# Kernel tuning notes

Hardware: AMD Instinct MI355X
Metric: run time of the kernel (lower is better)

## Reference

```python
import jax, jax.numpy as jnp
import numpy as np

B = 32768
N_INT = 32          # num_intruders
OWN_D = 3
INT_D = 7
ATTN_D = 128
HID = 256
OUT_D = 2
OBS_D = OWN_D + N_INT * INT_D  # 227
NEG_SLOPE = 0.2

def _lrelu(x):
    return jax.nn.leaky_relu(x, NEG_SLOPE)

def setup_inputs() -> dict:
    key = jax.random.key(0)
    ks = jax.random.split(key, 16)
    obs = jax.random.normal(ks[0], (B, OBS_D), dtype=jnp.float32)
    pad = jax.random.bernoulli(ks[1], 0.25, (B, N_INT))
    intr = obs[:, OWN_D:].reshape(B, N_INT, INT_D)
    intr = jnp.where(pad[:, :, None], 0.0, intr)
    obs = jnp.concatenate([obs[:, :OWN_D], intr.reshape(B, -1)], axis=1)
    def glorot(k, shape):
        fan_in, fan_out = shape[0], shape[-1]
        lim = jnp.sqrt(6.0 / (fan_in + fan_out))
        return jax.random.uniform(k, shape, jnp.float32, -lim, lim)
    return {
        "obs": obs,
        "own_W": glorot(ks[2], (OWN_D, ATTN_D)), "own_b": jnp.zeros((ATTN_D,), jnp.float32),
        "int_W": glorot(ks[3], (INT_D, ATTN_D)), "int_b": jnp.zeros((ATTN_D,), jnp.float32),
        "Wq": glorot(ks[4], (ATTN_D, ATTN_D)),
        "Wk": glorot(ks[5], (ATTN_D, ATTN_D)),
        "Wv": glorot(ks[6], (ATTN_D, ATTN_D)),
        "v_att": glorot(ks[7], (ATTN_D, 1))[:, 0],
        "proj_W": glorot(ks[8], (ATTN_D, ATTN_D)), "proj_b": jnp.zeros((ATTN_D,), jnp.float32),
        "h1_W": glorot(ks[9], (2 * ATTN_D, HID)), "h1_b": jnp.zeros((HID,), jnp.float32),
        "h2_W": glorot(ks[10], (HID, HID)), "h2_b": jnp.zeros((HID,), jnp.float32),
        "out_W": glorot(ks[11], (HID, OUT_D)), "out_b": jnp.zeros((OUT_D,), jnp.float32),
    }

def reference(obs, own_W, own_b, int_W, int_b, Wq, Wk, Wv, v_att,
              proj_W, proj_b, h1_W, h1_b, h2_W, h2_b, out_W, out_b):
    own = obs[:, :OWN_D]                                   # [B,3]
    intr = obs[:, OWN_D:OWN_D + N_INT * INT_D].reshape(-1, N_INT, INT_D)  # [B,N,7]
    own_e = _lrelu(own @ own_W + own_b)                    # [B,128]
    int_e = _lrelu(intr @ int_W + int_b)                   # [B,N,128]
    q = own_e @ Wq                                         # [B,128]
    k = int_e @ Wk                                         # [B,N,128]
    v = int_e @ Wv                                         # [B,N,128]
    energy = jnp.tanh(q[:, None, :] + k)                   # [B,N,128]
    scores = energy @ v_att                                # [B,N]
    is_padding = jnp.abs(intr).sum(axis=2) < 1e-6          # [B,N]
    scores = jnp.where(is_padding, -jnp.inf, scores)
    alpha = jax.nn.softmax(scores, axis=-1)
    alpha = jnp.nan_to_num(alpha, nan=0.0)
    ctx = jnp.einsum('bn,bnd->bd', alpha, v)               # [B,128]
    attn_vec = jnp.tanh(ctx @ proj_W + proj_b)             # [B,128]
    x = jnp.concatenate([own_e, attn_vec], axis=1)         # [B,256]
    x = _lrelu(x @ h1_W + h1_b)
    x = _lrelu(x @ h2_W + h2_b)
    return x @ out_W + out_b                               # [B,2]
```

## Files before the change

### kernel.cpp

```cpp
#include <hip/hip_runtime.h>
#include <hip/hip_bf16.h>
#include <math.h>

typedef _Float16 half2_t __attribute__((ext_vector_type(2)));
typedef _Float16 f16x8   __attribute__((ext_vector_type(8)));
typedef float    f32x4   __attribute__((ext_vector_type(4)));

constexpr int BATCH = 32768;
constexpr int NI   = 32;
constexpr int OWND = 3;
constexpr int INTD = 7;
constexpr int AD   = 128;
constexpr int HIDN = 256;
constexpr int OUTD = 2;
constexpr int OBSD = OWND + NI * INTD;
constexpr int IEPITCH = 68;
constexpr float C2L2E = 2.885390081777927f;

__device__ __forceinline__ half2_t u2h(unsigned u) { return __builtin_bit_cast(half2_t, u); }
__device__ __forceinline__ unsigned packf(float a, float b) {
    half2_t h = { (_Float16)a, (_Float16)b };
    return __builtin_bit_cast(unsigned, h);
}
__device__ __forceinline__ float lrelu(float x) { return fmaxf(x, 0.2f * x); }
__device__ __forceinline__ float exp2fast(float x) { return __builtin_amdgcn_exp2f(x); }
__device__ __forceinline__ float fast_tanh(float x) {
    float e = exp2fast(x * C2L2E);
    return 1.0f - 2.0f * __builtin_amdgcn_rcpf(e + 1.0f);
}

constexpr int UW_PWKQ = 0;
constexpr int UW_PWVF = 16384;
constexpr int UW_PPRF = 24576;
constexpr int UW_PIWF = 32768;
constexpr int UW_PH1F = 34816;
constexpr int UW_PH2F = 67584;
constexpr int UW_FULL = 100352;
constexpr size_t XBUF_U = (size_t)BATCH * (HIDN / 2);

__global__ __launch_bounds__(256) void pack_full(
    const float* __restrict__ Wq, const float* __restrict__ Wk,
    const float* __restrict__ Wv, const float* __restrict__ Pr,
    const float* __restrict__ IW, const float* __restrict__ IB,
    const float* __restrict__ H1, const float* __restrict__ H2,
    unsigned* __restrict__ dst)
{
    int u = blockIdx.x * 256 + threadIdx.x;
    if (u >= UW_FULL) return;
    if (u < 16384) {
        int f = u >> 8, kt = f >> 3, nt = f & 7;
        int idx = u & 255, lane = idx >> 2, w = idx & 3;
        int qd = lane >> 4, lo = lane & 15;
        const float* src = (kt < 4) ? Wk : Wq;
        int ktp = kt & 3;
        int r0 = 32 * ktp + 8 * qd + 2 * w, col = 16 * nt + lo;
        dst[u] = packf(src[r0 * 128 + col], src[(r0 + 1) * 128 + col]);
    } else if (u < 32768) {
        const float* src = (u < 24576) ? Wv : Pr;
        int i = (u - 16384) & 8191;
        int f = i >> 8, kt = f >> 3, nt = f & 7;
        int idx = i & 255, lane = idx >> 2, w = idx & 3;
        int qd = lane >> 4, lo = lane & 15;
        int r0 = 32 * kt + 8 * qd + 2 * w, col = 16 * nt + lo;
        dst[u] = packf(src[r0 * 128 + col], src[(r0 + 1) * 128 + col]);
    } else if (u < 34816) {
        int i = u - 32768;
        int nt = i >> 8;
        int idx = i & 255, lane = idx >> 2, w = idx & 3;
        int qd = lane >> 4, lo = lane & 15;
        int r0 = 8 * qd + 2 * w, col = 16 * nt + lo;
        float v0 = (r0 < INTD) ? IW[r0 * 128 + col] : 0.f;
        float v1 = (r0 + 1 < INTD) ? IW[(r0 + 1) * 128 + col]
                 : ((r0 + 1 == INTD) ? IB[col] : 0.f);
        dst[u] = packf(v0, v1);
    } else {
        int i = u - 34816;
        const float* src = (i < 32768) ? H1 : H2;
        i &= 32767;
        int f = i >> 8, nt = f >> 3, kt = f & 7;
        int idx = i & 255, lane = idx >> 2, w = idx & 3;
        int qd = lane >> 4, lo = lane & 15;
        int r0 = 32 * kt + 8 * qd + 2 * w, col = 16 * nt + lo;
        dst[u] = packf(src[r0 * 256 + col], src[(r0 + 1) * 256 + col]);
    }
}

__global__ __launch_bounds__(256) void qgemm(
    const float* __restrict__ obs, const float* __restrict__ own_W,
    const float* __restrict__ own_b, const unsigned* __restrict__ pWkqF,
    float* __restrict__ qall)
{
    const int wv = threadIdx.x >> 6;
    const int l  = threadIdx.x & 63;
    const int lo = l & 15, qd = l >> 4;
    const size_t row0 = (size_t)blockIdx.x * 64 + (size_t)wv * 16;

    __shared__ __align__(16) float    s_own[4][16][4];
    __shared__ __align__(16) unsigned s_oe[4][16 * 68];

    if (l < 16) {
        const float* orow = obs + (row0 + l) * OBSD;
        s_own[wv][l][0] = orow[0]; s_own[wv][l][1] = orow[1]; s_own[wv][l][2] = orow[2];
    }

    {
        const float x0 = s_own[wv][lo][0], x1 = s_own[wv][lo][1], x2 = s_own[wv][lo][2];
        #pragma unroll
        for (int jj = 0; jj < 8; jj++) {
            const int c4 = qd * 32 + jj * 4;
            float4 wb = *(const float4*)(own_b + c4);
            float4 w0 = *(const float4*)(own_W + 0 * AD + c4);
            float4 w1 = *(const float4*)(own_W + 1 * AD + c4);
            float4 w2 = *(const float4*)(own_W + 2 * AD + c4);
            float v0 = lrelu(wb.x + x0 * w0.x + x1 * w1.x + x2 * w2.x);
            float v1 = lrelu(wb.y + x0 * w0.y + x1 * w1.y + x2 * w2.y);
            float v2 = lrelu(wb.z + x0 * w0.z + x1 * w1.z + x2 * w2.z);
            float v3 = lrelu(wb.w + x0 * w0.w + x1 * w1.w + x2 * w2.w);
            s_oe[wv][lo * 68 + (c4 >> 1)]     = packf(v0, v1);
            s_oe[wv][lo * 68 + (c4 >> 1) + 1] = packf(v2, v3);
        }
    }

    f16x8 aE[4];
    #pragma unroll
    for (int kt = 0; kt < 4; kt++) {
        uint4 au = *(const uint4*)(&s_oe[wv][lo * 68 + 16 * kt + 4 * qd]);
        aE[kt] = __builtin_bit_cast(f16x8, au);
    }
    #pragma unroll
    for (int nt = 0; nt < 8; nt++) {
        f32x4 acc = {0.f, 0.f, 0.f, 0.f};
        #pragma unroll
        for (int kt = 0; kt < 4; kt++) {
            uint4 bu = *(const uint4*)(pWkqF + (((kt + 4) * 8 + nt) << 8) + (l << 2));
            acc = __builtin_amdgcn_mfma_f32_16x16x32_f16(aE[kt], __builtin_bit_cast(f16x8, bu), acc, 0, 0, 0);
        }
        #pragma unroll
        for (int r = 0; r < 4; r++)
            qall[(row0 + 4 * qd + r) * AD + 16 * nt + lo] = acc[r];
    }
}

__global__ __launch_bounds__(256) void attn(
    const float* __restrict__ obs,
    const float* __restrict__ own_W, const float* __restrict__ own_b,
    const unsigned* __restrict__ pIWF, const float* __restrict__ int_b,
    const unsigned* __restrict__ pWkqF, const float* __restrict__ v_att,
    const float* __restrict__ qall,
    unsigned* __restrict__ xbuf)
{
    const int wv = threadIdx.x >> 6;
    const int l  = threadIdx.x & 63;
    const int b  = blockIdx.x * 4 + wv;
    const int d0 = 2 * l;
    const int lo = l & 15, qd = l >> 4;
    const bool useQ = (qall != nullptr);

    __shared__ __align__(16) unsigned s_w[10240];
    __shared__ __align__(16) float    s_obs[4][OBSD];
    __shared__ __align__(16) unsigned s_ieb[4][NI * IEPITCH];
    __shared__ __align__(16) unsigned s_ownh[4][AD / 2];
    __shared__ __align__(16) float    s_sc[4][NI];

    if (useQ) {
        #pragma unroll
        for (int it = 0; it < 8; it++) {
            int idx = (threadIdx.x + it * 256) << 2;
            *(uint4*)(&s_w[idx]) = *(const uint4*)(pWkqF + idx);
        }
        #pragma unroll
        for (int it = 0; it < 2; it++) {
            int idx = (threadIdx.x + it * 256) << 2;
            *(uint4*)(&s_w[8192 + idx]) = *(const uint4*)(pIWF + idx);
        }
    }

    const float* orow = obs + (size_t)b * OBSD;
    for (int i = l; i < OBSD; i += 64) s_obs[wv][i] = orow[i];

    float oe0 = own_b[d0], oe1 = own_b[d0 + 1];
    #pragma unroll
    for (int j = 0; j < OWND; j++) {
        float x = s_obs[wv][j];
        oe0 += x * own_W[j * AD + d0];
        oe1 += x * own_W[j * AD + d0 + 1];
    }
    oe0 = lrelu(oe0); oe1 = lrelu(oe1);
    s_ownh[wv][l] = packf(oe0, oe1);

    int padf = 0;
    if (l < NI) {
        float su = 0.f;
        #pragma unroll
        for (int j = 0; j < INTD; j++) su += fabsf(s_obs[wv][OWND + l * INTD + j]);
        padf = (su < 1e-6f);
    }

    float qe[8];
    if (useQ) {
        const float* qrow = qall + (size_t)b * AD;
        #pragma unroll
        for (int nt = 0; nt < 8; nt++) qe[nt] = qrow[16 * nt + lo] * C2L2E;
    } else {
        #pragma unroll
        for (int nt = 0; nt < 8; nt++) qe[nt] = 0.f;
    }

    f16x8 aInt[2];
    #pragma unroll
    for (int t = 0; t < 2; t++) {
        #pragma unroll
        for (int j = 0; j < 8; j++) {
            int k = 8 * qd + j;
            float v;
            if (k < INTD)       v = s_obs[wv][OWND + (16 * t + lo) * INTD + k];
            else if (k == INTD) v = 1.0f;
            else                v = 0.f;
            aInt[t][j] = (_Float16)v;
        }
    }

    if (useQ) __syncthreads();

    _Float16* s_ieh = (_Float16*)s_ieb[wv];
    #pragma unroll
    for (int nt = 0; nt < 8; nt++) {
        uint4 bu;
        if (useQ) bu = *(const uint4*)(&s_w[8192 + (nt << 8) + (l << 2)]);
        else      bu = *(const uint4*)(pIWF + (nt << 8) + (l << 2));
        f16x8 bf = __builtin_bit_cast(f16x8, bu);
        f32x4 z = {0.f, 0.f, 0.f, 0.f};
        f32x4 c0 = __builtin_amdgcn_mfma_f32_16x16x32_f16(aInt[0], bf, z, 0, 0, 0);
        f32x4 c1 = __builtin_amdgcn_mfma_f32_16x16x32_f16(aInt[1], bf, z, 0, 0, 0);
        const int cswz = (16 * nt + lo) ^ (qd << 3);
        #pragma unroll
        for (int r = 0; r < 4; r++) {
            s_ieh[(4 * qd + r) * 136 + cswz]      = (_Float16)lrelu(c0[r]);
            s_ieh[(16 + 4 * qd + r) * 136 + cswz] = (_Float16)lrelu(c1[r]);
        }
    }

    const int slo = ((lo >> 2) & 3) << 2;
    f16x8 aIE[2][4];
    #pragma unroll
    for (int t = 0; t < 2; t++)
        #pragma unroll
        for (int kt = 0; kt < 4; kt++) {
            uint4 au = *(const uint4*)(&s_ieb[wv][(16 * t + lo) * IEPITCH + ((16 * kt + 4 * qd) ^ slo)]);
            aIE[t][kt] = __builtin_bit_cast(f16x8, au);
        }

    float sA0[4] = {0.f, 0.f, 0.f, 0.f};
    float sA1[4] = {0.f, 0.f, 0.f, 0.f};
    float vsum = 0.f;
    #pragma unroll
    for (int nt = 0; nt < 8; nt++) {
        f32x4 acc0 = {0.f, 0.f, 0.f, 0.f};
        f32x4 acc1 = {0.f, 0.f, 0.f, 0.f};
        if (useQ) {
            #pragma unroll
            for (int kt = 0; kt < 4; kt++) {
                uint4 bu = *(const uint4*)(&s_w[((kt * 8 + nt) << 8) + (l << 2)]);
                f16x8 bf = __builtin_bit_cast(f16x8, bu);
                acc0 = __builtin_amdgcn_mfma_f32_16x16x32_f16(aIE[0][kt], bf, acc0, 0, 0, 0);
                acc1 = __builtin_amdgcn_mfma_f32_16x16x32_f16(aIE[1][kt], bf, acc1, 0, 0, 0);
            }
        } else {
            #pragma unroll
            for (int kt = 0; kt < 8; kt++) {
                uint4 bu = *(const uint4*)(pWkqF + ((kt * 8 + nt) << 8) + (l << 2));
                f16x8 bf = __builtin_bit_cast(f16x8, bu);
                f16x8 af0, af1;
                if (kt < 4) { af0 = aIE[0][kt]; af1 = aIE[1][kt]; }
                else {
                    uint4 au = *(const uint4*)(&s_ownh[wv][16 * (kt - 4) + 4 * qd]);
                    af0 = __builtin_bit_cast(f16x8, au);
                    af1 = af0;
                }
                acc0 = __builtin_amdgcn_mfma_f32_16x16x32_f16(af0, bf, acc0, 0, 0, 0);
                acc1 = __builtin_amdgcn_mfma_f32_16x16x32_f16(af1, bf, acc1, 0, 0, 0);
            }
        }
        const float vc   = v_att[16 * nt + lo];
        const float n2vc = -2.0f * vc;
        vsum += vc;
        #pragma unroll
        for (int r = 0; r < 4; r++) {
            float t0 = exp2fast(fmaf(acc0[r], C2L2E, qe[nt]));
            sA0[r] = fmaf(n2vc, __builtin_amdgcn_rcpf(t0 + 1.0f), sA0[r]);
            float t1 = exp2fast(fmaf(acc1[r], C2L2E, qe[nt]));
            sA1[r] = fmaf(n2vc, __builtin_amdgcn_rcpf(t1 + 1.0f), sA1[r]);
        }
    }
    #pragma unroll
    for (int r = 0; r < 4; r++) { sA0[r] += vsum; sA1[r] += vsum; }
    #pragma unroll
    for (int r = 0; r < 4; r++) {
        #pragma unroll
        for (int w = 1; w <= 8; w <<= 1) {
            sA0[r] += __shfl_xor(sA0[r], w, 64);
            sA1[r] += __shfl_xor(sA1[r], w, 64);
        }
    }
    if (lo == 0) {
        #pragma unroll
        for (int r = 0; r < 4; r++) {
            s_sc[wv][4 * qd + r]      = sA0[r];
            s_sc[wv][16 + 4 * qd + r] = sA1[r];
        }
    }

    {
        float sval = -INFINITY;
        if (l < NI && !padf) sval = s_sc[wv][l];
        float mm = sval;
        #pragma unroll
        for (int w = 1; w <= 16; w <<= 1) mm = fmaxf(mm, __shfl_xor(mm, w, 64));
        float e = (sval > -INFINITY) ? __expf(sval - mm) : 0.f;
        float dd = e;
        #pragma unroll
        for (int w = 1; w <= 16; w <<= 1) dd += __shfl_xor(dd, w, 64);
        if (l < NI) s_sc[wv][l] = (dd > 0.f) ? e * __builtin_amdgcn_rcpf(dd) : 0.f;
    }

    float sv0 = 0.f, sv1 = 0.f;
    #pragma unroll
    for (int n = 0; n < NI; n++) {
        const int sn = ((n >> 2) & 3) << 2;
        half2_t ie = u2h(s_ieb[wv][n * IEPITCH + (l ^ sn)]);
        float a = s_sc[wv][n];
        sv0 += a * (float)ie.x; sv1 += a * (float)ie.y;
    }
    xbuf[(size_t)b * (HIDN / 2) + l]      = s_ownh[wv][l];
    xbuf[(size_t)b * (HIDN / 2) + 64 + l] = packf(sv0, sv1);
}

__global__ __launch_bounds__(256) void mlp32(
    const unsigned* __restrict__ xbuf,
    const unsigned* __restrict__ pWvF, const float* __restrict__ proj_b,
    const unsigned* __restrict__ pPrF,
    const unsigned* __restrict__ pH1F, const float* __restrict__ h1_b,
    const unsigned* __restrict__ pH2F, const float* __restrict__ h2_b,
    const float* __restrict__ out_W,   const float* __restrict__ out_b,
    float* __restrict__ res)
{
    const int tid = threadIdx.x;
    const int wv  = tid >> 6;
    const int l   = tid & 63;
    const int lo  = l & 15, qd = l >> 4;
    const size_t row0 = (size_t)blockIdx.x * 32;

    __shared__ __align__(16) unsigned s_x[32 * 132];
    __shared__ __align__(16) unsigned s_scr[32 * 68];
    __shared__ __align__(16) float    s_red[4][32][2];

    #pragma unroll
    for (int it = 0; it < 4; it++) {
        int i = tid + it * 256;
        int r = i >> 5, cq = i & 31;
        uint4 u = *(const uint4*)(xbuf + (row0 + r) * 128 + cq * 4);
        if (cq < 16) *(uint4*)(&s_x[r * 132 + cq * 4]) = u;
        else         *(uint4*)(&s_scr[r * 68 + (cq - 16) * 4]) = u;
    }
    __syncthreads();

    _Float16* s_ctxh = (_Float16*)s_scr;
    _Float16* s_xh   = (_Float16*)s_x;

    #pragma unroll
    for (int rowg = 0; rowg < 2; rowg++) {
        const int rb = 16 * rowg;
        f16x8 aS[4];
        #pragma unroll
        for (int kt = 0; kt < 4; kt++) {
            uint4 au = *(const uint4*)(&s_scr[(rb + lo) * 68 + 16 * kt + 4 * qd]);
            aS[kt] = __builtin_bit_cast(f16x8, au);
        }
        __syncthreads();
        #pragma unroll
        for (int ni = 0; ni < 2; ni++) {
            const int nt = 2 * wv + ni;
            f32x4 acc = {0.f, 0.f, 0.f, 0.f};
            #pragma unroll
            for (int kt = 0; kt < 4; kt++) {
                uint4 bu = *(const uint4*)(pWvF + ((kt * 8 + nt) << 8) + (l << 2));
                acc = __builtin_amdgcn_mfma_f32_16x16x32_f16(aS[kt], __builtin_bit_cast(f16x8, bu), acc, 0, 0, 0);
            }
            #pragma unroll
            for (int r = 0; r < 4; r++)
                s_ctxh[(rb + 4 * qd + r) * 136 + 16 * nt + lo] = (_Float16)acc[r];
        }
    }
    __syncthreads();

    #pragma unroll
    for (int rowg = 0; rowg < 2; rowg++) {
        const int rb = 16 * rowg;
        f16x8 aC[4];
        #pragma unroll
        for (int kt = 0; kt < 4; kt++) {
            uint4 au = *(const uint4*)(&s_scr[(rb + lo) * 68 + 16 * kt + 4 * qd]);
            aC[kt] = __builtin_bit_cast(f16x8, au);
        }
        #pragma unroll
        for (int ni = 0; ni < 2; ni++) {
            const int nt = 2 * wv + ni;
            f32x4 acc = {0.f, 0.f, 0.f, 0.f};
            #pragma unroll
            for (int kt = 0; kt < 4; kt++) {
                uint4 bu = *(const uint4*)(pPrF + ((kt * 8 + nt) << 8) + (l << 2));
                acc = __builtin_amdgcn_mfma_f32_16x16x32_f16(aC[kt], __builtin_bit_cast(f16x8, bu), acc, 0, 0, 0);
            }
            const float bn = proj_b[16 * nt + lo];
            #pragma unroll
            for (int r = 0; r < 4; r++)
                s_xh[(rb + 4 * qd + r) * 264 + 128 + 16 * nt + lo] = (_Float16)fast_tanh(acc[r] + bn);
        }
    }
    __syncthreads();

    {
        f16x8 aX[8];
        #pragma unroll
        for (int kt = 0; kt < 8; kt++) {
            uint4 au = *(const uint4*)(&s_x[lo * 132 + 16 * kt + 4 * qd]);
            aX[kt] = __builtin_bit_cast(f16x8, au);
        }
        __syncthreads();
        #pragma unroll
        for (int ni = 0; ni < 4; ni++) {
            const int nt = 4 * wv + ni;
            f32x4 acc = {0.f, 0.f, 0.f, 0.f};
            #pragma unroll
            for (int kt = 0; kt < 8; kt++) {
                uint4 bu = *(const uint4*)(pH1F + ((nt * 8 + kt) << 8) + (l << 2));
                acc = __builtin_amdgcn_mfma_f32_16x16x32_f16(aX[kt], __builtin_bit_cast(f16x8, bu), acc, 0, 0, 0);
            }
            const float bn = h1_b[16 * nt + lo];
            #pragma unroll
            for (int r = 0; r < 4; r++)
                s_xh[(4 * qd + r) * 264 + 16 * nt + lo] = (_Float16)lrelu(acc[r] + bn);
        }
        #pragma unroll
        for (int kt = 0; kt < 8; kt++) {
            uint4 au = *(const uint4*)(&s_x[(16 + lo) * 132 + 16 * kt + 4 * qd]);
            aX[kt] = __builtin_bit_cast(f16x8, au);
        }
        __syncthreads();
        #pragma unroll
        for (int ni = 0; ni < 4; ni++) {
            const int nt = 4 * wv + ni;
            f32x4 acc = {0.f, 0.f, 0.f, 0.f};
            #pragma unroll
            for (int kt = 0; kt < 8; kt++) {
                uint4 bu = *(const uint4*)(pH1F + ((nt * 8 + kt) << 8) + (l << 2));
                acc = __builtin_amdgcn_mfma_f32_16x16x32_f16(aX[kt], __builtin_bit_cast(f16x8, bu), acc, 0, 0, 0);
            }
            const float bn = h1_b[16 * nt + lo];
            #pragma unroll
            for (int r = 0; r < 4; r++)
                s_xh[(16 + 4 * qd + r) * 264 + 16 * nt + lo] = (_Float16)lrelu(acc[r] + bn);
        }
    }
    __syncthreads();

    #pragma unroll
    for (int rowg = 0; rowg < 2; rowg++) {
        const int rb = 16 * rowg;
        f16x8 aH[8];
        #pragma unroll
        for (int kt = 0; kt < 8; kt++) {
            uint4 au = *(const uint4*)(&s_x[(rb + lo) * 132 + 16 * kt + 4 * qd]);
            aH[kt] = __builtin_bit_cast(f16x8, au);
        }
        float o0[4] = {0.f, 0.f, 0.f, 0.f};
        float o1[4] = {0.f, 0.f, 0.f, 0.f};
        #pragma unroll
        for (int ni = 0; ni < 4; ni++) {
            const int nt = 4 * wv + ni;
            f32x4 acc = {0.f, 0.f, 0.f, 0.f};
            #pragma unroll
            for (int kt = 0; kt < 8; kt++) {
                uint4 bu = *(const uint4*)(pH2F + ((nt * 8 + kt) << 8) + (l << 2));
                acc = __builtin_amdgcn_mfma_f32_16x16x32_f16(aH[kt], __builtin_bit_cast(f16x8, bu), acc, 0, 0, 0);
            }
            const float bn = h2_b[16 * nt + lo];
            float2 w = *(const float2*)(out_W + (size_t)(16 * nt + lo) * OUTD);
            #pragma unroll
            for (int r = 0; r < 4; r++) {
                float v = lrelu(acc[r] + bn);
                o0[r] += v * w.x; o1[r] += v * w.y;
            }
        }
        #pragma unroll
        for (int r = 0; r < 4; r++) {
            #pragma unroll
            for (int w = 1; w <= 8; w <<= 1) {
                o0[r] += __shfl_xor(o0[r], w, 64);
                o1[r] += __shfl_xor(o1[r], w, 64);
            }
        }
        if (lo == 0) {
            #pragma unroll
            for (int r = 0; r < 4; r++) {
                s_red[wv][rb + 4 * qd + r][0] = o0[r];
                s_red[wv][rb + 4 * qd + r][1] = o1[r];
            }
        }
    }
    __syncthreads();
    if (tid < 64) {
        int r = tid >> 1, cmp = tid & 1;
        float s = s_red[0][r][cmp] + s_red[1][r][cmp]
                + s_red[2][r][cmp] + s_red[3][r][cmp] + out_b[cmp];
        res[(row0 + r) * OUTD + cmp] = s;
    }
}

__global__ __launch_bounds__(256) void copy_out(const float* __restrict__ src,
                                               float* __restrict__ dst, int n4) {
    int i = blockIdx.x * 256 + threadIdx.x;
    if (i < n4) ((float4*)dst)[i] = ((const float4*)src)[i];
}

extern "C" void kernel_launch(void* const* d_in, const int* in_sizes, int n_in,
                              void* d_out, int out_size, void* d_ws, size_t ws_size,
                              hipStream_t stream) {
    const float* obs    = (const float*)d_in[0];
    const float* own_W  = (const float*)d_in[1];
    const float* own_b  = (const float*)d_in[2];
    const float* int_W  = (const float*)d_in[3];
    const float* int_b  = (const float*)d_in[4];
    const float* Wq     = (const float*)d_in[5];
    const float* Wk     = (const float*)d_in[6];
    const float* Wv     = (const float*)d_in[7];
    const float* v_att  = (const float*)d_in[8];
    const float* proj_W = (const float*)d_in[9];
    const float* proj_b = (const float*)d_in[10];
    const float* h1_W   = (const float*)d_in[11];
    const float* h1_b   = (const float*)d_in[12];
    const float* h2_W   = (const float*)d_in[13];
    const float* h2_b   = (const float*)d_in[14];
    const float* out_W  = (const float*)d_in[15];
    const float* out_b  = (const float*)d_in[16];

    const size_t res_bytes  = (size_t)BATCH * OUTD * sizeof(float);
    const size_t q_bytes    = (size_t)BATCH * AD * sizeof(float);
    const size_t base_bytes = (size_t)UW_FULL * 4 + XBUF_U * 4 + res_bytes;
    const int n4 = BATCH * OUTD / 4;

    if (ws_size >= base_bytes + q_bytes) {
        unsigned* pw   = (unsigned*)d_ws;
        unsigned* xbuf = pw + UW_FULL;
        float*    qall = (float*)(xbuf + XBUF_U);
        float*    res  = qall + (size_t)BATCH * AD;
        pack_full<<<(UW_FULL + 255) / 256, 256, 0, stream>>>(
            Wq, Wk, Wv, proj_W, int_W, int_b, h1_W, h2_W, pw);
        qgemm<<<BATCH / 64, 256, 0, stream>>>(obs, own_W, own_b, pw + UW_PWKQ, qall);
        attn<<<BATCH / 4, 256, 0, stream>>>(
            obs, own_W, own_b, pw + UW_PIWF, int_b,
            pw + UW_PWKQ, v_att, qall, xbuf);
        mlp32<<<BATCH / 32, 256, 0, stream>>>(
            xbuf, pw + UW_PWVF, proj_b, pw + UW_PPRF,
            pw + UW_PH1F, h1_b, pw + UW_PH2F, h2_b, out_W, out_b, res);
        copy_out<<<(n4 + 255) / 256, 256, 0, stream>>>(res, (float*)d_out, n4);
    } else if (ws_size >= base_bytes) {
        unsigned* pw   = (unsigned*)d_ws;
        unsigned* xbuf = pw + UW_FULL;
        float*    res  = (float*)(xbuf + XBUF_U);
        pack_full<<<(UW_FULL + 255) / 256, 256, 0, stream>>>(
            Wq, Wk, Wv, proj_W, int_W, int_b, h1_W, h2_W, pw);
        attn<<<BATCH / 4, 256, 0, stream>>>(
            obs, own_W, own_b, pw + UW_PIWF, int_b,
            pw + UW_PWKQ, v_att, nullptr, xbuf);
        mlp32<<<BATCH / 32, 256, 0, stream>>>(
            xbuf, pw + UW_PWVF, proj_b, pw + UW_PPRF,
            pw + UW_PH1F, h1_b, pw + UW_PH2F, h2_b, out_W, out_b, res);
        copy_out<<<(n4 + 255) / 256, 256, 0, stream>>>(res, (float*)d_out, n4);
    }
}
```

Baseline: 277.4 us.

## Read attn weights from global instead of LDS; use 8 waves in MLP kernel

The attention kernel stops staging the 40 KB of packed Wk/int_W weights into shared memory per block and drops the block-wide barrier, reading the B-fragments straight from global/L2 instead. This lowers LDS use so more blocks fit per CU, at the cost of repeated global loads. The MLP kernel is relaunched with 512 threads (8 waves), and each wave now computes fewer output tiles, which adds parallelism per block and needs an 8-way final reduction.

Measured after the change: 238.6 us. 14.0% less time.

```diff
diff --git a/kernel.cpp b/kernel.cpp
--- a/kernel.cpp
+++ b/kernel.cpp
@@ -156,24 +156,10 @@
     const int lo = l & 15, qd = l >> 4;
     const bool useQ = (qall != nullptr);
 
-    __shared__ __align__(16) unsigned s_w[10240];
     __shared__ __align__(16) float    s_obs[4][OBSD];
     __shared__ __align__(16) unsigned s_ieb[4][NI * IEPITCH];
     __shared__ __align__(16) unsigned s_ownh[4][AD / 2];
     __shared__ __align__(16) float    s_sc[4][NI];
-
-    if (useQ) {
-        #pragma unroll
-        for (int it = 0; it < 8; it++) {
-            int idx = (threadIdx.x + it * 256) << 2;
-            *(uint4*)(&s_w[idx]) = *(const uint4*)(pWkqF + idx);
-        }
-        #pragma unroll
-        for (int it = 0; it < 2; it++) {
-            int idx = (threadIdx.x + it * 256) << 2;
-            *(uint4*)(&s_w[8192 + idx]) = *(const uint4*)(pIWF + idx);
-        }
-    }
 
     const float* orow = obs + (size_t)b * OBSD;
     for (int i = l; i < OBSD; i += 64) s_obs[wv][i] = orow[i];
@@ -219,15 +205,10 @@
             aInt[t][j] = (_Float16)v;
         }
     }
-
-    if (useQ) __syncthreads();
-
     _Float16* s_ieh = (_Float16*)s_ieb[wv];
     #pragma unroll
     for (int nt = 0; nt < 8; nt++) {
-        uint4 bu;
-        if (useQ) bu = *(const uint4*)(&s_w[8192 + (nt << 8) + (l << 2)]);
-        else      bu = *(const uint4*)(pIWF + (nt << 8) + (l << 2));
+        uint4 bu = *(const uint4*)(pIWF + (nt << 8) + (l << 2));
         f16x8 bf = __builtin_bit_cast(f16x8, bu);
         f32x4 z = {0.f, 0.f, 0.f, 0.f};
         f32x4 c0 = __builtin_amdgcn_mfma_f32_16x16x32_f16(aInt[0], bf, z, 0, 0, 0);
@@ -260,7 +241,7 @@
         if (useQ) {
             #pragma unroll
             for (int kt = 0; kt < 4; kt++) {
-                uint4 bu = *(const uint4*)(&s_w[((kt * 8 + nt) << 8) + (l << 2)]);
+                uint4 bu = *(const uint4*)(pWkqF + ((kt * 8 + nt) << 8) + (l << 2));
                 f16x8 bf = __builtin_bit_cast(f16x8, bu);
                 acc0 = __builtin_amdgcn_mfma_f32_16x16x32_f16(aIE[0][kt], bf, acc0, 0, 0, 0);
                 acc1 = __builtin_amdgcn_mfma_f32_16x16x32_f16(aIE[1][kt], bf, acc1, 0, 0, 0);
@@ -335,7 +316,7 @@
     xbuf[(size_t)b * (HIDN / 2) + 64 + l] = packf(sv0, sv1);
 }
 
-__global__ __launch_bounds__(256) void mlp32(
+__global__ __launch_bounds__(512) void mlp8w(
     const unsigned* __restrict__ xbuf,
     const unsigned* __restrict__ pWvF, const float* __restrict__ proj_b,
     const unsigned* __restrict__ pPrF,
@@ -352,11 +333,11 @@
 
     __shared__ __align__(16) unsigned s_x[32 * 132];
     __shared__ __align__(16) unsigned s_scr[32 * 68];
-    __shared__ __align__(16) float    s_red[4][32][2];
-
-    #pragma unroll
-    for (int it = 0; it < 4; it++) {
-        int i = tid + it * 256;
+    __shared__ __align__(16) float    s_red[8][32][2];
+
+    #pragma unroll
+    for (int it = 0; it < 2; it++) {
+        int i = tid + it * 512;
         int r = i >> 5, cq = i & 31;
         uint4 u = *(const uint4*)(xbuf + (row0 + r) * 128 + cq * 4);
         if (cq < 16) *(uint4*)(&s_x[r * 132 + cq * 4]) = u;
@@ -377,61 +358,79 @@
             aS[kt] = __builtin_bit_cast(f16x8, au);
         }
         __syncthreads();
+        {
+            const int nt = wv;
+            f32x4 acc = {0.f, 0.f, 0.f, 0.f};
+            #pragma unroll
+            for (int kt = 0; kt < 4; kt++) {
+                uint4 bu = *(const uint4*)(pWvF + ((kt * 8 + nt) << 8) + (l << 2));
+                acc = __builtin_amdgcn_mfma_f32_16x16x32_f16(aS[kt], __builtin_bit_cast(f16x8, bu), acc, 0, 0, 0);
+            }
+            #pragma unroll
+            for (int r = 0; r < 4; r++)
+                s_ctxh[(rb + 4 * qd + r) * 136 + 16 * nt + lo] = (_Float16)acc[r];
+        }
+    }
+    __syncthreads();
+
+    #pragma unroll
+    for (int rowg = 0; rowg < 2; rowg++) {
+        const int rb = 16 * rowg;
+        f16x8 aC[4];
+        #pragma unroll
+        for (int kt = 0; kt < 4; kt++) {
+            uint4 au = *(const uint4*)(&s_scr[(rb + lo) * 68 + 16 * kt + 4 * qd]);
+            aC[kt] = __builtin_bit_cast(f16x8, au);
+        }
+        {
+            const int nt = wv;
+            f32x4 acc = {0.f, 0.f, 0.f, 0.f};
+            #pragma unroll
+            for (int kt = 0; kt < 4; kt++) {
+                uint4 bu = *(const uint4*)(pPrF + ((kt * 8 + nt) << 8) + (l << 2));
+                acc = __builtin_amdgcn_mfma_f32_16x16x32_f16(aC[kt], __builtin_bit_cast(f16x8, bu), acc, 0, 0, 0);
+            }
+            const float bn = proj_b[16 * nt + lo];
+            #pragma unroll
+            for (int r = 0; r < 4; r++)
+                s_xh[(rb + 4 * qd + r) * 264 + 128 + 16 * nt + lo] = (_Float16)fast_tanh(acc[r] + bn);
+        }
+    }
+    __syncthreads();
+
+    {
+        f16x8 aX[8];
+        #pragma unroll
+        for (int kt = 0; kt < 8; kt++) {
+            uint4 au = *(const uint4*)(&s_x[lo * 132 + 16 * kt + 4 * qd]);
+            aX[kt] = __builtin_bit_cast(f16x8, au);
+        }
+        __syncthreads();
         #pragma unroll
         for (int ni = 0; ni < 2; ni++) {
             const int nt = 2 * wv + ni;
             f32x4 acc = {0.f, 0.f, 0.f, 0.f};
             #pragma unroll
-            for (int kt = 0; kt < 4; kt++) {
-                uint4 bu = *(const uint4*)(pWvF + ((kt * 8 + nt) << 8) + (l << 2));
-                acc = __builtin_amdgcn_mfma_f32_16x16x32_f16(aS[kt], __builtin_bit_cast(f16x8, bu), acc, 0, 0, 0);
-            }
+            for (int kt = 0; kt < 8; kt++) {
+                uint4 bu = *(const uint4*)(pH1F + ((nt * 8 + kt) << 8) + (l << 2));
+                acc = __builtin_amdgcn_mfma_f32_16x16x32_f16(aX[kt], __builtin_bit_cast(f16x8, bu), acc, 0, 0, 0);
+            }
+            const float bn = h1_b[16 * nt + lo];
             #pragma unroll
             for (int r = 0; r < 4; r++)
-                s_ctxh[(rb + 4 * qd + r) * 136 + 16 * nt + lo] = (_Float16)acc[r];
-        }
-    }
-    __syncthreads();
-
-    #pragma unroll
-    for (int rowg = 0; rowg < 2; rowg++) {
-        const int rb = 16 * rowg;
-        f16x8 aC[4];
-        #pragma unroll
-        for (int kt = 0; kt < 4; kt++) {
-            uint4 au = *(const uint4*)(&s_scr[(rb + lo) * 68 + 16 * kt + 4 * qd]);
-            aC[kt] = __builtin_bit_cast(f16x8, au);
-        }
+                s_xh[(4 * qd + r) * 264 + 16 * nt + lo] = (_Float16)lrelu(acc[r] + bn);
+        }
+        #pragma unroll
+        for (int kt = 0; kt < 8; kt++) {
+            uint4 au = *(const uint4*)(&s_x[(16 + lo) * 132 + 16 * kt + 4 * qd]);
+            aX[kt] = __builtin_bit_cast(f16x8, au);
+        }
+        __syncthreads();
         #pragma unroll
         for (int ni = 0; ni < 2; ni++) {
             const int nt = 2 * wv + ni;
             f32x4 acc = {0.f, 0.f, 0.f, 0.f};
             #pragma unroll
-            for (int kt = 0; kt < 4; kt++) {
-                uint4 bu = *(const uint4*)(pPrF + ((kt * 8 + nt) << 8) + (l << 2));
-                acc = __builtin_amdgcn_mfma_f32_16x16x32_f16(aC[kt], __builtin_bit_cast(f16x8, bu), acc, 0, 0, 0);
-            }
-            const float bn = proj_b[16 * nt + lo];
-            #pragma unroll
-            for (int r = 0; r < 4; r++)
-                s_xh[(rb + 4 * qd + r) * 264 + 128 + 16 * nt + lo] = (_Float16)fast_tanh(acc[r] + bn);
-        }
-    }
-    __syncthreads();
-
-    {
-        f16x8 aX[8];
-        #pragma unroll
-        for (int kt = 0; kt < 8; kt++) {
-            uint4 au = *(const uint4*)(&s_x[lo * 132 + 16 * kt + 4 * qd]);
-            aX[kt] = __builtin_bit_cast(f16x8, au);
-        }
-        __syncthreads();
-        #pragma unroll
-        for (int ni = 0; ni < 4; ni++) {
-            const int nt = 4 * wv + ni;
-            f32x4 acc = {0.f, 0.f, 0.f, 0.f};
-            #pragma unroll
             for (int kt = 0; kt < 8; kt++) {
                 uint4 bu = *(const uint4*)(pH1F + ((nt * 8 + kt) << 8) + (l << 2));
                 acc = __builtin_amdgcn_mfma_f32_16x16x32_f16(aX[kt], __builtin_bit_cast(f16x8, bu), acc, 0, 0, 0);
@@ -439,26 +438,6 @@
             const float bn = h1_b[16 * nt + lo];
             #pragma unroll
             for (int r = 0; r < 4; r++)
-                s_xh[(4 * qd + r) * 264 + 16 * nt + lo] = (_Float16)lrelu(acc[r] + bn);
-        }
-        #pragma unroll
-        for (int kt = 0; kt < 8; kt++) {
-            uint4 au = *(const uint4*)(&s_x[(16 + lo) * 132 + 16 * kt + 4 * qd]);
-            aX[kt] = __builtin_bit_cast(f16x8, au);
-        }
-        __syncthreads();
-        #pragma unroll
-        for (int ni = 0; ni < 4; ni++) {
-            const int nt = 4 * wv + ni;
-            f32x4 acc = {0.f, 0.f, 0.f, 0.f};
-            #pragma unroll
-            for (int kt = 0; kt < 8; kt++) {
-                uint4 bu = *(const uint4*)(pH1F + ((nt * 8 + kt) << 8) + (l << 2));
-                acc = __builtin_amdgcn_mfma_f32_16x16x32_f16(aX[kt], __builtin_bit_cast(f16x8, bu), acc, 0, 0, 0);
-            }
-            const float bn = h1_b[16 * nt + lo];
-            #pragma unroll
-            for (int r = 0; r < 4; r++)
                 s_xh[(16 + 4 * qd + r) * 264 + 16 * nt + lo] = (_Float16)lrelu(acc[r] + bn);
         }
     }
@@ -476,8 +455,8 @@
         float o0[4] = {0.f, 0.f, 0.f, 0.f};
         float o1[4] = {0.f, 0.f, 0.f, 0.f};
         #pragma unroll
-        for (int ni = 0; ni < 4; ni++) {
-            const int nt = 4 * wv + ni;
+        for (int ni = 0; ni < 2; ni++) {
+            const int nt = 2 * wv + ni;
             f32x4 acc = {0.f, 0.f, 0.f, 0.f};
             #pragma unroll
             for (int kt = 0; kt < 8; kt++) {
@@ -511,8 +490,9 @@
     __syncthreads();
     if (tid < 64) {
         int r = tid >> 1, cmp = tid & 1;
-        float s = s_red[0][r][cmp] + s_red[1][r][cmp]
-                + s_red[2][r][cmp] + s_red[3][r][cmp] + out_b[cmp];
+        float s = out_b[cmp];
+        #pragma unroll
+        for (int w = 0; w < 8; w++) s += s_red[w][r][cmp];
         res[(row0 + r) * OUTD + cmp] = s;
     }
 }
@@ -560,7 +540,7 @@
         attn<<<BATCH / 4, 256, 0, stream>>>(
             obs, own_W, own_b, pw + UW_PIWF, int_b,
             pw + UW_PWKQ, v_att, qall, xbuf);
-        mlp32<<<BATCH / 32, 256, 0, stream>>>(
+        mlp8w<<<BATCH / 32, 512, 0, stream>>>(
             xbuf, pw + UW_PWVF, proj_b, pw + UW_PPRF,
             pw + UW_PH1F, h1_b, pw + UW_PH2F, h2_b, out_W, out_b, res);
         copy_out<<<(n4 + 255) / 256, 256, 0, stream>>>(res, (float*)d_out, n4);
@@ -573,7 +553,7 @@
         attn<<<BATCH / 4, 256, 0, stream>>>(
             obs, own_W, own_b, pw + UW_PIWF, int_b,
             pw + UW_PWKQ, v_att, nullptr, xbuf);
-        mlp32<<<BATCH / 32, 256, 0, stream>>>(
+        mlp8w<<<BATCH / 32, 512, 0, stream>>>(
             xbuf, pw + UW_PWVF, proj_b, pw + UW_PPRF,
             pw + UW_PH1F, h1_b, pw + UW_PH2F, h2_b, out_W, out_b, res);
         copy_out<<<(n4 + 255) / 256, 256, 0, stream>>>(res, (float*)d_out, n4);
```
